# Kernel tuning notes

Hardware: AMD Instinct MI355X
Metric: run time of the kernel (lower is better)

Reference implementation:

```python
import jax, jax.numpy as jnp
import numpy as np

N_NODES = 100000
N_EDGES = 1200000
D_IN = 64
D_OUT = 64


def setup_inputs() -> dict:
    key = jax.random.key(0)
    ks = jax.random.split(key, 8)
    feat = jax.random.normal(ks[0], (N_NODES, D_IN), dtype=jnp.float32)
    src = jax.random.randint(ks[1], (N_EDGES,), 0, N_NODES, dtype=jnp.int32)
    dst = jax.random.randint(ks[2], (N_EDGES,), 0, N_NODES, dtype=jnp.int32)
    edge_weight = jax.random.uniform(ks[3], (N_EDGES, 1), dtype=jnp.float32)
    edge_mask = jax.random.uniform(ks[4], (N_EDGES, 1), dtype=jnp.float32)
    W_self = jax.random.normal(ks[5], (D_OUT, D_IN), dtype=jnp.float32) * (1.0 / np.sqrt(D_IN))
    b_self = jnp.zeros((D_OUT,), dtype=jnp.float32)
    W_neigh = jax.random.normal(ks[6], (D_OUT, D_IN), dtype=jnp.float32) * (1.0 / np.sqrt(D_IN))
    b_neigh = jnp.zeros((D_OUT,), dtype=jnp.float32)
    return {"feat": feat, "src": src, "dst": dst, "edge_weight": edge_weight,
            "edge_mask": edge_mask, "W_self": W_self, "b_self": b_self,
            "W_neigh": W_neigh, "b_neigh": b_neigh}


def reference(feat, src, dst, edge_weight, edge_mask, W_self, b_self, W_neigh, b_neigh):
    # message: gather src feats, scale by per-edge weight and mask  -> [E, D_IN]
    msg = feat[src] * edge_weight * edge_mask
    # mean scatter-reduce over incoming edges per dst node
    neigh_sum = jax.ops.segment_sum(msg, dst, num_segments=N_NODES)  # [N, D_IN]
    deg = jax.ops.segment_sum(jnp.ones((msg.shape[0],), dtype=feat.dtype), dst,
                              num_segments=N_NODES)  # [N]
    h_neigh = neigh_sum / jnp.maximum(deg, 1.0)[:, None]  # zero-degree nodes -> 0 (DGL mean semantics)
    # dual linear fuse
    rst = (feat @ W_self.T + b_self) + (h_neigh @ W_neigh.T + b_neigh)
    return rst
```

## Files before the change

### kernel.cpp

```cpp
#include <hip/hip_runtime.h>

#define NB_MAX   1568
#define CAP      1024
#define BT_EDGES 4096
#define BT_TPB   1024
#define EPE      4

typedef __attribute__((ext_vector_type(4))) float floatx4;
typedef __attribute__((ext_vector_type(2))) float floatx2;
typedef __attribute__((ext_vector_type(8))) short bf16x8;

__device__ __forceinline__ unsigned short f32_to_bf16(float f) {
  unsigned u = __float_as_uint(f);
  u = (u + 0x7fffu + ((u >> 16) & 1u)) >> 16;
  return (unsigned short)u;
}
__device__ __forceinline__ unsigned pack2(float a, float b) {
  return (unsigned)f32_to_bf16(a) | ((unsigned)f32_to_bf16(b) << 16);
}
__device__ __forceinline__ bf16x8 zero_bf16x8() {
  bf16x8 v;
#pragma unroll
  for (int i = 0; i < 8; ++i) v[i] = 0;
  return v;
}

#if __has_builtin(__builtin_amdgcn_cvt_pk_fp8_f32)
__device__ __forceinline__ unsigned pack_fp8x4(float a, float b, float c, float d) {
  unsigned v = (unsigned)__builtin_amdgcn_cvt_pk_fp8_f32(a, b, 0, false);
  v = (unsigned)__builtin_amdgcn_cvt_pk_fp8_f32(c, d, (int)v, true);
  return v;
}
#else
__device__ __forceinline__ unsigned sw_f32_fp8(float f) {
  unsigned u = __float_as_uint(f);
  unsigned s = (u >> 24) & 0x80u;
  unsigned au = u & 0x7fffffffu;
  if (au > 0x43E00000u) au = 0x43E00000u;
  au += 0x7FFFFu + ((au >> 20) & 1u);
  int e = (int)(au >> 23) - 120;
  if (e <= 0) return s;
  return s | ((unsigned)e << 3) | ((au >> 20) & 7u);
}
__device__ __forceinline__ unsigned pack_fp8x4(float a, float b, float c, float d) {
  return sw_f32_fp8(a) | (sw_f32_fp8(b) << 8) | (sw_f32_fp8(c) << 16) |
         (sw_f32_fp8(d) << 24);
}
#endif

#if __has_builtin(__builtin_amdgcn_cvt_pk_f32_fp8)
__device__ __forceinline__ void dec4(float* acc, unsigned w32, float wt) {
  floatx2 f0 = __builtin_amdgcn_cvt_pk_f32_fp8((int)w32, false);
  floatx2 f1 = __builtin_amdgcn_cvt_pk_f32_fp8((int)w32, true);
  acc[0] += wt * f0.x; acc[1] += wt * f0.y;
  acc[2] += wt * f1.x; acc[3] += wt * f1.y;
}
#else
__device__ __forceinline__ float sw_fp8_f32(unsigned b) {
  unsigned s = (b & 0x80u) << 24;
  unsigned e = (b >> 3) & 0xFu;
  unsigned m = b & 7u;
  float fn = __uint_as_float(s | ((e + 120u) << 23) | (m << 20));
  float fd = (float)(int)m * 0.001953125f;
  fd = (b & 0x80u) ? -fd : fd;
  return e ? fn : fd;
}
__device__ __forceinline__ void dec4(float* acc, unsigned w32, float wt) {
  acc[0] += wt * sw_fp8_f32(w32 & 0xFF);
  acc[1] += wt * sw_fp8_f32((w32 >> 8) & 0xFF);
  acc[2] += wt * sw_fp8_f32((w32 >> 16) & 0xFF);
  acc[3] += wt * sw_fp8_f32(w32 >> 24);
}
#endif

__global__ __launch_bounds__(BT_TPB) void k_build(
    const float* __restrict__ feat, const int* __restrict__ src,
    const int* __restrict__ dst, const float* __restrict__ ew,
    const float* __restrict__ em, const float* __restrict__ Ws,
    const float* __restrict__ Wn, int* __restrict__ gCursor,
    unsigned* __restrict__ recs, unsigned short* __restrict__ featb,
    unsigned char* __restrict__ featq, unsigned short* __restrict__ Wb,
    int E, int nChunks, int nB) {
  __shared__ unsigned stage[BT_EDGES];
  __shared__ unsigned short stageB[BT_EDGES];
  __shared__ int A[NB_MAX];
  __shared__ int B[NB_MAX];
  __shared__ int waveSums[16];

  const int t = threadIdx.x;
  const int lane = t & 63;
  const int wvid = t >> 6;
  const int e0 = blockIdx.x * BT_EDGES;
  const int eEnd = min(e0 + BT_EDGES, E);
  const int nLocal = eEnd - e0;

  for (int i = t; i < NB_MAX; i += BT_TPB) B[i] = 0;
  __syncthreads();

  int dreg[EPE];
#pragma unroll
  for (int k = 0; k < EPE; ++k) {
    int i = e0 + k * BT_TPB + t;
    dreg[k] = -1;
    if (i < eEnd) {
      int d = dst[i];
      dreg[k] = d;
      atomicAdd(&B[d >> 6], 1);
    }
  }
  __syncthreads();

  {
    const int EPT = 2;
    int b0 = t * EPT;
    int v[EPT];
    int sum = 0;
#pragma unroll
    for (int j = 0; j < EPT; ++j) {
      v[j] = (b0 + j < nB) ? B[b0 + j] : 0;
      sum += v[j];
    }
    int x = sum;
#pragma unroll
    for (int d = 1; d < 64; d <<= 1) {
      int y = __shfl_up(x, d, 64);
      if (lane >= d) x += y;
    }
    if (lane == 63) waveSums[wvid] = x;
    __syncthreads();
    int wprefix = 0;
    for (int i = 0; i < wvid; ++i) wprefix += waveSums[i];
    int run = wprefix + x - sum;
#pragma unroll
    for (int j = 0; j < EPT; ++j) {
      if (b0 + j < nB) A[b0 + j] = run;
      run += v[j];
    }
  }
  __syncthreads();

  for (int i = t; i < nB; i += BT_TPB) {
    int c = B[i];
    int l = A[i];
    int g = c ? atomicAdd(&gCursor[i], c) : 0;
    A[i] = i * CAP + g - l;
    B[i] = l;
  }
  __syncthreads();

#pragma unroll
  for (int k = 0; k < EPE; ++k) {
    int i = e0 + k * BT_TPB + t;
    if (i < eEnd) {
      int d = dreg[k];
      int bkt = d >> 6;
      int r = atomicAdd(&B[bkt], 1);
      float w = ew[i] * em[i];
      int wq = (int)(w * 511.0f + 0.5f);
      if (wq > 511) wq = 511;
      stage[r] = (unsigned)src[i] | ((unsigned)(d & 63) << 17) |
                 ((unsigned)wq << 23);
      stageB[r] = (unsigned short)bkt;
    }
  }
  __syncthreads();

  for (int i = t; i < nLocal; i += BT_TPB) {
    int bkt = stageB[i];
    int pos = A[bkt] + i;
    if (pos < (bkt + 1) * CAP)
      recs[pos] = stage[i];
  }

  for (int c = blockIdx.x * BT_TPB + t; c < nChunks; c += gridDim.x * BT_TPB) {
    const float4* fp = reinterpret_cast<const float4*>(feat) + (size_t)c * 2;
    float4 a = fp[0], b = fp[1];
    uint4 o;
    o.x = pack2(a.x, a.y);
    o.y = pack2(a.z, a.w);
    o.z = pack2(b.x, b.y);
    o.w = pack2(b.z, b.w);
    reinterpret_cast<uint4*>(featb)[c] = o;
    uint2 q8;
    q8.x = pack_fp8x4(a.x, a.y, a.z, a.w);
    q8.y = pack_fp8x4(b.x, b.y, b.z, b.w);
    reinterpret_cast<uint2*>(featq)[c] = q8;
  }

  if (blockIdx.x == 0) {
    for (int i = t; i < 1024; i += BT_TPB) {
      int j = i >> 4, c4 = i & 15;
      float4 w4 = reinterpret_cast<const float4*>(Ws)[i];
      float4 n4 = reinterpret_cast<const float4*>(Wn)[i];
      *reinterpret_cast<uint2*>(&Wb[j * 128 + c4 * 4]) =
          make_uint2(pack2(w4.x, w4.y), pack2(w4.z, w4.w));
      *reinterpret_cast<uint2*>(&Wb[j * 128 + 64 + c4 * 4]) =
          make_uint2(pack2(n4.x, n4.y), pack2(n4.z, n4.w));
    }
  }
}

__global__ __launch_bounds__(512) void sage_gather_gemm(
    const unsigned short* __restrict__ featb,
    const unsigned char* __restrict__ featq,
    const unsigned short* __restrict__ Wb, const int* __restrict__ gCursor,
    const unsigned* __restrict__ recs, const float* __restrict__ bs,
    const float* __restrict__ bn, float* __restrict__ out, int N) {
  __shared__ unsigned short An[64][72];
  __shared__ unsigned rawL[CAP];
  __shared__ unsigned srtL[CAP];
  __shared__ float pf[64][64];
  __shared__ int cntS[64], offS[64], curS[64];

  const int t = threadIdx.x;
  const int b = blockIdx.x;
  const int n0 = b * 64;
  const int base = b * CAP;
  const int cb = min(gCursor[b], CAP);

  for (int i = t; i < cb; i += 512) rawL[i] = recs[base + i];
  if (t < 64) cntS[t] = 0;
  __syncthreads();

  for (int i = t; i < cb; i += 512)
    atomicAdd(&cntS[(rawL[i] >> 17) & 63], 1);
  __syncthreads();

  if (t < 64) {
    int c = cntS[t];
    int x = c;
#pragma unroll
    for (int d = 1; d < 64; d <<= 1) {
      int y = __shfl_up(x, d, 64);
      if (t >= d) x += y;
    }
    offS[t] = x - c;
    curS[t] = x - c;
  }
  __syncthreads();

  for (int i = t; i < cb; i += 512) {
    unsigned r = rawL[i];
    int p = atomicAdd(&curS[(r >> 17) & 63], 1);
    srtL[p] = r;
  }
  __syncthreads();

  {
    const int nl = t >> 3;
    const int g  = (t >> 2) & 1;
    const int q  = t & 3;
    const int deg = cntS[nl], off = offS[nl];
    const int myN = (deg - g + 1) >> 1;
    float acc[16];
#pragma unroll
    for (int i = 0; i < 16; ++i) acc[i] = 0.f;
    const uint4* fq = reinterpret_cast<const uint4*>(featq);

    uint4 uC, uN;
    float wC = 0.f, wN = 0.f;
    if (myN > 0) {
      unsigned r0 = srtL[off + g];
      uC = fq[(size_t)(r0 & 0x1FFFF) * 4 + q];
      wC = (float)(r0 >> 23) * (1.0f / 511.0f);
    }
    if (myN > 1) {
      unsigned r1 = srtL[off + g + 2];
      uN = fq[(size_t)(r1 & 0x1FFFF) * 4 + q];
      wN = (float)(r1 >> 23) * (1.0f / 511.0f);
    }
    for (int m = 0; m < myN; ++m) {
      uint4 u = uC;
      float w = wC;
      uC = uN; wC = wN;
      if (m + 2 < myN) {
        unsigned rn = srtL[off + g + 2 * (m + 2)];
        uN = fq[(size_t)(rn & 0x1FFFF) * 4 + q];
        wN = (float)(rn >> 23) * (1.0f / 511.0f);
      }
      dec4(acc + 0, u.x, w);
      dec4(acc + 4, u.y, w);
      dec4(acc + 8, u.z, w);
      dec4(acc + 12, u.w, w);
    }

    if (g == 1) {
#pragma unroll
      for (int i = 0; i < 16; ++i) pf[nl][q * 16 + i] = acc[i];
    }
    __syncthreads();
    if (g == 0) {
      float inv = 1.0f / fmaxf((float)deg, 1.0f);
#pragma unroll
      for (int i = 0; i < 16; ++i) acc[i] = (acc[i] + pf[nl][q * 16 + i]) * inv;
      uint4 o0, o1;
      o0.x = pack2(acc[0], acc[1]);
      o0.y = pack2(acc[2], acc[3]);
      o0.z = pack2(acc[4], acc[5]);
      o0.w = pack2(acc[6], acc[7]);
      o1.x = pack2(acc[8], acc[9]);
      o1.y = pack2(acc[10], acc[11]);
      o1.z = pack2(acc[12], acc[13]);
      o1.w = pack2(acc[14], acc[15]);
      *reinterpret_cast<uint4*>(&An[nl][q * 16]) = o0;
      *reinterpret_cast<uint4*>(&An[nl][q * 16 + 8]) = o1;
    }
  }
  __syncthreads();

  const int wv8 = t >> 6;
  const int nt = wv8 & 3;
  const int jh = wv8 >> 2;
  const int ln = t & 63;
  const int col = ln & 15;
  const int quad = ln >> 4;
  const int gn = n0 + nt * 16 + col;

  floatx4 acc4[2];
#pragma unroll
  for (int jj = 0; jj < 2; ++jj) {
    int jt = jh * 2 + jj;
    float bb = bs[jt * 16 + col] + bn[jt * 16 + col];
    acc4[jj] = (floatx4){bb, bb, bb, bb};
  }

#pragma unroll
  for (int kk = 0; kk < 4; ++kk) {
    bf16x8 af;
    if (kk < 2) {
      if (gn < N) {
        af = *reinterpret_cast<const bf16x8*>(featb + (size_t)gn * 64 + kk * 32 + quad * 8);
      } else {
        af = zero_bf16x8();
      }
    } else {
      af = *reinterpret_cast<const bf16x8*>(&An[nt * 16 + col][(kk - 2) * 32 + quad * 8]);
    }
#pragma unroll
    for (int jj = 0; jj < 2; ++jj) {
      int jt = jh * 2 + jj;
      bf16x8 bf = *reinterpret_cast<const bf16x8*>(
          Wb + (jt * 16 + col) * 128 + kk * 32 + quad * 8);
      acc4[jj] = __builtin_amdgcn_mfma_f32_16x16x32_bf16(af, bf, acc4[jj], 0, 0, 0);
    }
  }

#pragma unroll
  for (int jj = 0; jj < 2; ++jj) {
    int jt = jh * 2 + jj;
#pragma unroll
    for (int r = 0; r < 4; ++r) {
      int m = quad * 4 + r;
      int g2 = n0 + nt * 16 + m;
      if (g2 < N) out[(size_t)g2 * 64 + jt * 16 + col] = acc4[jj][r];
    }
  }
}

extern "C" void kernel_launch(void* const* d_in, const int* in_sizes, int n_in,
                              void* d_out, int out_size, void* d_ws, size_t ws_size,
                              hipStream_t stream) {
  const float* feat = (const float*)d_in[0];
  const int*   src  = (const int*)d_in[1];
  const int*   dst  = (const int*)d_in[2];
  const float* ew   = (const float*)d_in[3];
  const float* em   = (const float*)d_in[4];
  const float* Ws   = (const float*)d_in[5];
  const float* bs   = (const float*)d_in[6];
  const float* Wn   = (const float*)d_in[7];
  const float* bn   = (const float*)d_in[8];
  float* out = (float*)d_out;

  const int N = in_sizes[0] / 64;
  const int E = in_sizes[1];
  const int nB = (N + 63) / 64;

  unsigned short* featb = (unsigned short*)d_ws;
  unsigned char*  featq = (unsigned char*)(featb + (size_t)N * 64);
  unsigned short* Wb    = (unsigned short*)(featq + (size_t)N * 64);
  unsigned* recs   = (unsigned*)(Wb + 64 * 128);
  int*      gCursor = (int*)(recs + (size_t)NB_MAX * CAP);

  hipMemsetAsync(gCursor, 0, NB_MAX * sizeof(int), stream);

  int nChunks = N * 8;
  int gB = (E + BT_EDGES - 1) / BT_EDGES;

  k_build<<<gB, BT_TPB, 0, stream>>>(feat, src, dst, ew, em, Ws, Wn,
                                     gCursor, recs, featb, featq, Wb,
                                     E, nChunks, nB);
  sage_gather_gemm<<<nB, 512, 0, stream>>>(featb, featq, Wb, gCursor, recs,
                                           bs, bn, out, N);
}
```

Baseline: 158.4 us.

## Use nontemporal loads/stores, shuffle-reduce partials, prefetch self features early

Makes global loads and stores of edge arrays, features, records and output nontemporal. The second gather kernel now combines its two partial sums with a cross-lane shuffle instead of a shared-memory array plus a barrier, and fuses the record copy with the degree counting. It also issues the self-feature and bias loads before the gather phase so their latency overlaps the sort and gather. The binning kernel handles 5120 edges per block instead of 4096, which holds more per-thread state in registers.

```diff
diff --git a/kernel.cpp b/kernel.cpp
--- a/kernel.cpp
+++ b/kernel.cpp
@@ -2,13 +2,14 @@
 
 #define NB_MAX   1568
 #define CAP      1024
-#define BT_EDGES 4096
+#define BT_EDGES 5120
 #define BT_TPB   1024
-#define EPE      4
+#define EPE      5
 
 typedef __attribute__((ext_vector_type(4))) float floatx4;
 typedef __attribute__((ext_vector_type(2))) float floatx2;
 typedef __attribute__((ext_vector_type(8))) short bf16x8;
+typedef __attribute__((ext_vector_type(4))) unsigned uintx4;
 
 __device__ __forceinline__ unsigned short f32_to_bf16(float f) {
   unsigned u = __float_as_uint(f);
@@ -103,7 +104,7 @@
     int i = e0 + k * BT_TPB + t;
     dreg[k] = -1;
     if (i < eEnd) {
-      int d = dst[i];
+      int d = __builtin_nontemporal_load(&dst[i]);
       dreg[k] = d;
       atomicAdd(&B[d >> 6], 1);
     }
@@ -155,11 +156,12 @@
       int d = dreg[k];
       int bkt = d >> 6;
       int r = atomicAdd(&B[bkt], 1);
-      float w = ew[i] * em[i];
+      float w = __builtin_nontemporal_load(&ew[i]) *
+                __builtin_nontemporal_load(&em[i]);
       int wq = (int)(w * 511.0f + 0.5f);
       if (wq > 511) wq = 511;
-      stage[r] = (unsigned)src[i] | ((unsigned)(d & 63) << 17) |
-                 ((unsigned)wq << 23);
+      stage[r] = (unsigned)__builtin_nontemporal_load(&src[i]) |
+                 ((unsigned)(d & 63) << 17) | ((unsigned)wq << 23);
       stageB[r] = (unsigned short)bkt;
     }
   }
@@ -173,14 +175,15 @@
   }
 
   for (int c = blockIdx.x * BT_TPB + t; c < nChunks; c += gridDim.x * BT_TPB) {
-    const float4* fp = reinterpret_cast<const float4*>(feat) + (size_t)c * 2;
-    float4 a = fp[0], b = fp[1];
-    uint4 o;
+    const floatx4* fp = reinterpret_cast<const floatx4*>(feat) + (size_t)c * 2;
+    floatx4 a = __builtin_nontemporal_load(fp);
+    floatx4 b = __builtin_nontemporal_load(fp + 1);
+    uintx4 o;
     o.x = pack2(a.x, a.y);
     o.y = pack2(a.z, a.w);
     o.z = pack2(b.x, b.y);
     o.w = pack2(b.z, b.w);
-    reinterpret_cast<uint4*>(featb)[c] = o;
+    __builtin_nontemporal_store(o, reinterpret_cast<uintx4*>(featb) + c);
     uint2 q8;
     q8.x = pack_fp8x4(a.x, a.y, a.z, a.w);
     q8.y = pack_fp8x4(b.x, b.y, b.z, b.w);
@@ -209,7 +212,6 @@
   __shared__ unsigned short An[64][72];
   __shared__ unsigned rawL[CAP];
   __shared__ unsigned srtL[CAP];
-  __shared__ float pf[64][64];
   __shared__ int cntS[64], offS[64], curS[64];
 
   const int t = threadIdx.x;
@@ -218,12 +220,31 @@
   const int base = b * CAP;
   const int cb = min(gCursor[b], CAP);
 
-  for (int i = t; i < cb; i += 512) rawL[i] = recs[base + i];
   if (t < 64) cntS[t] = 0;
   __syncthreads();
 
-  for (int i = t; i < cb; i += 512)
-    atomicAdd(&cntS[(rawL[i] >> 17) & 63], 1);
+  for (int i = t; i < cb; i += 512) {
+    unsigned r = __builtin_nontemporal_load(&recs[base + i]);
+    rawL[i] = r;
+    atomicAdd(&cntS[(r >> 17) & 63], 1);
+  }
+
+  const int wv8 = t >> 6;
+  const int ntile = wv8 & 3;
+  const int jh = wv8 >> 2;
+  const int ln = t & 63;
+  const int col = ln & 15;
+  const int quad = ln >> 4;
+  const int gn = n0 + ntile * 16 + col;
+  bf16x8 af0 = zero_bf16x8(), af1 = zero_bf16x8();
+  if (gn < N) {
+    af0 = __builtin_nontemporal_load(
+        reinterpret_cast<const bf16x8*>(featb + (size_t)gn * 64 + quad * 8));
+    af1 = __builtin_nontemporal_load(
+        reinterpret_cast<const bf16x8*>(featb + (size_t)gn * 64 + 32 + quad * 8));
+  }
+  const float bb0 = bs[(jh * 2) * 16 + col] + bn[(jh * 2) * 16 + col];
+  const float bb1 = bs[(jh * 2 + 1) * 16 + col] + bn[(jh * 2 + 1) * 16 + col];
   __syncthreads();
 
   if (t < 64) {
@@ -257,7 +278,7 @@
     for (int i = 0; i < 16; ++i) acc[i] = 0.f;
     const uint4* fq = reinterpret_cast<const uint4*>(featq);
 
-    uint4 uC, uN;
+    uint4 uC = {0, 0, 0, 0}, uN = {0, 0, 0, 0};
     float wC = 0.f, wN = 0.f;
     if (myN > 0) {
       unsigned r0 = srtL[off + g];
@@ -284,15 +305,13 @@
       dec4(acc + 12, u.w, w);
     }
 
-    if (g == 1) {
-#pragma unroll
-      for (int i = 0; i < 16; ++i) pf[nl][q * 16 + i] = acc[i];
-    }
-    __syncthreads();
+#pragma unroll
+    for (int i = 0; i < 16; ++i) acc[i] += __shfl_xor(acc[i], 4, 64);
+
     if (g == 0) {
       float inv = 1.0f / fmaxf((float)deg, 1.0f);
 #pragma unroll
-      for (int i = 0; i < 16; ++i) acc[i] = (acc[i] + pf[nl][q * 16 + i]) * inv;
+      for (int i = 0; i < 16; ++i) acc[i] *= inv;
       uint4 o0, o1;
       o0.x = pack2(acc[0], acc[1]);
       o0.y = pack2(acc[2], acc[3]);
@@ -308,34 +327,18 @@
   }
   __syncthreads();
 
-  const int wv8 = t >> 6;
-  const int nt = wv8 & 3;
-  const int jh = wv8 >> 2;
-  const int ln = t & 63;
-  const int col = ln & 15;
-  const int quad = ln >> 4;
-  const int gn = n0 + nt * 16 + col;
-
   floatx4 acc4[2];
-#pragma unroll
-  for (int jj = 0; jj < 2; ++jj) {
-    int jt = jh * 2 + jj;
-    float bb = bs[jt * 16 + col] + bn[jt * 16 + col];
-    acc4[jj] = (floatx4){bb, bb, bb, bb};
-  }
+  acc4[0] = (floatx4){bb0, bb0, bb0, bb0};
+  acc4[1] = (floatx4){bb1, bb1, bb1, bb1};
 
 #pragma unroll
   for (int kk = 0; kk < 4; ++kk) {
     bf16x8 af;
-    if (kk < 2) {
-      if (gn < N) {
-        af = *reinterpret_cast<const bf16x8*>(featb + (size_t)gn * 64 + kk * 32 + quad * 8);
-      } else {
-        af = zero_bf16x8();
-      }
-    } else {
-      af = *reinterpret_cast<const bf16x8*>(&An[nt * 16 + col][(kk - 2) * 32 + quad * 8]);
-    }
+    if (kk == 0)      af = af0;
+    else if (kk == 1) af = af1;
+    else
+      af = *reinterpret_cast<const bf16x8*>(
+          &An[ntile * 16 + col][(kk - 2) * 32 + quad * 8]);
 #pragma unroll
     for (int jj = 0; jj < 2; ++jj) {
       int jt = jh * 2 + jj;
@@ -351,8 +354,10 @@
 #pragma unroll
     for (int r = 0; r < 4; ++r) {
       int m = quad * 4 + r;
-      int g2 = n0 + nt * 16 + m;
-      if (g2 < N) out[(size_t)g2 * 64 + jt * 16 + col] = acc4[jj][r];
+      int g2 = n0 + ntile * 16 + m;
+      if (g2 < N)
+        __builtin_nontemporal_store(acc4[jj][r],
+                                    &out[(size_t)g2 * 64 + jt * 16 + col]);
     }
   }
 }
```

Measured after the change: 159.1 us. About the same (+0.5%).
